# Optimization experiments

Measured on AMD Instinct MI355X. Metric: run time of the kernel, lower is better.

## Reference

```python
import jax, jax.numpy as jnp
import numpy as np

FACTOR = 8
IN_DIM = 4096
OUT_DIM = 4096


def setup_inputs() -> dict:
    key = jax.random.key(0)
    kx, ka, ks = jax.random.split(key, 3)
    x = jax.random.normal(kx, (4, 2048, IN_DIM), dtype=jnp.float32)
    a = jax.random.normal(ka, (FACTOR, FACTOR, FACTOR), dtype=jnp.float32) * 0.1
    s = jax.random.normal(ks, (FACTOR, OUT_DIM // FACTOR, IN_DIM // FACTOR), dtype=jnp.float32) * 0.05
    return {"x": x, "a": a, "s": s}


def reference(x, a, s):
    f = a.shape[0]
    out_dim = a.shape[1] * s.shape[1]
    in_dim = a.shape[2] * s.shape[2]
    # Batched Kronecker product: (f, a_rows*k, a_cols*p) then sum over batch dim f.
    # weight[a*k + ?, c*p + ?] = sum_b a[b, ar, ac] * s[b, kr, pc]
    p = jnp.einsum('bac,bkp->bakcp', a, s)  # (f, f, out/f, f, in/f)
    weight = p.reshape(f, out_dim, in_dim).sum(axis=0)  # (out, in)
    return x @ weight.T
```

## Files before the change

### kernel.cpp

```cpp
#include <hip/hip_runtime.h>
#include <hip/hip_bf16.h>
#include <stdint.h>

namespace {

constexpr int MTOT = 8192;
constexpr int NTOT = 4096;
constexpr int KTOT = 4096;

constexpr int BM = 256, BN = 128, BK = 32;
constexpr int NT = KTOT / BK;

typedef __attribute__((ext_vector_type(8))) short bf16x8;
typedef __attribute__((ext_vector_type(4))) float f32x4;

__device__ inline unsigned short to_bf16(float f) {
    union { float f; uint32_t u; } v; v.f = f;
    return (unsigned short)((v.u + 0x7FFFu + ((v.u >> 16) & 1u)) >> 16);
}

__global__ __launch_bounds__(256) void convert_x_kernel(const float* __restrict__ x,
                                                        unsigned short* __restrict__ xb) {
    int idx = blockIdx.x * 256 + threadIdx.x;
    const f32x4* xv = reinterpret_cast<const f32x4*>(x);
    f32x4 v0 = xv[2 * idx];
    f32x4 v1 = xv[2 * idx + 1];
    union { bf16x8 v; unsigned short s[8]; } o;
    o.s[0] = to_bf16(v0.x); o.s[1] = to_bf16(v0.y);
    o.s[2] = to_bf16(v0.z); o.s[3] = to_bf16(v0.w);
    o.s[4] = to_bf16(v1.x); o.s[5] = to_bf16(v1.y);
    o.s[6] = to_bf16(v1.z); o.s[7] = to_bf16(v1.w);
    reinterpret_cast<bf16x8*>(xb)[idx] = o.v;
}

__global__ __launch_bounds__(256) void gen_w_kernel(const float* __restrict__ a,
                                                    const float* __restrict__ s,
                                                    unsigned short* __restrict__ w) {
    int idx = blockIdx.x * 256 + threadIdx.x;
    int o  = idx >> 9;
    int i8 = idx & 511;
    int i0 = i8 * 8;
    int obig = o >> 9, orow = o & 511;
    int ibig = i0 >> 9, icol = i0 & 511;

    float acc[8];
#pragma unroll
    for (int j = 0; j < 8; ++j) acc[j] = 0.f;

#pragma unroll
    for (int b = 0; b < 8; ++b) {
        float av = a[b * 64 + obig * 8 + ibig];
        const f32x4* sv = reinterpret_cast<const f32x4*>(s + b * 512 * 512 + orow * 512 + icol);
        f32x4 s0 = sv[0], s1 = sv[1];
        acc[0] += av * s0.x; acc[1] += av * s0.y; acc[2] += av * s0.z; acc[3] += av * s0.w;
        acc[4] += av * s1.x; acc[5] += av * s1.y; acc[6] += av * s1.z; acc[7] += av * s1.w;
    }
    union { bf16x8 v; unsigned short q[8]; } ov;
#pragma unroll
    for (int j = 0; j < 8; ++j) ov.q[j] = to_bf16(acc[j]);
    reinterpret_cast<bf16x8*>(w)[idx] = ov.v;
}

__global__ __launch_bounds__(256, 2)
void gemm_bt_kernel(const unsigned short* __restrict__ A,
                    const unsigned short* __restrict__ B,
                    float* __restrict__ C) {
    __shared__ __align__(16) unsigned short As[3][BM][BK];
    __shared__ __align__(16) unsigned short Bs[3][BN][BK];

    int bid = blockIdx.x;
    int swz = (bid & 7) * 128 + (bid >> 3);
    int bm = swz >> 5;
    int bn = swz & 31;

    int tid  = threadIdx.x;
    int wid  = tid >> 6;
    int lane = tid & 63;
    int wm = wid >> 1, wn = wid & 1;

    int srow  = lane >> 2;
    int sslot = (lane & 3) ^ ((srow >> 1) & 3);
    const unsigned short* ag = A + (size_t)(bm * BM + wid * 64 + srow) * KTOT + sslot * 8;
    const unsigned short* bg = B + (size_t)(bn * BN + wid * 32 + srow) * KTOT + sslot * 8;

    int rl    = lane & 15;
    int rslot = (lane >> 4) ^ ((rl >> 1) & 3);

    f32x4 acc[8][4];
#pragma unroll
    for (int m = 0; m < 8; ++m)
#pragma unroll
        for (int n = 0; n < 4; ++n) acc[m][n] = (f32x4)0.f;

    auto STAGE = [&](int s, int k0) {
#pragma unroll
        for (int g = 0; g < 4; ++g)
            __builtin_amdgcn_global_load_lds(
                (const __attribute__((address_space(1))) void*)(ag + (size_t)g * 16 * KTOT + k0),
                (__attribute__((address_space(3))) void*)&As[s][wid * 64 + g * 16][0], 16, 0, 0);
#pragma unroll
        for (int g = 0; g < 2; ++g)
            __builtin_amdgcn_global_load_lds(
                (const __attribute__((address_space(1))) void*)(bg + (size_t)g * 16 * KTOT + k0),
                (__attribute__((address_space(3))) void*)&Bs[s][wid * 32 + g * 16][0], 16, 0, 0);
    };

    auto COMPUTE = [&](int s) {
        bf16x8 fa[8], fb[4];
#pragma unroll
        for (int m = 0; m < 8; ++m)
            fa[m] = *reinterpret_cast<const bf16x8*>(&As[s][wm * 128 + m * 16 + rl][rslot * 8]);
#pragma unroll
        for (int n = 0; n < 4; ++n)
            fb[n] = *reinterpret_cast<const bf16x8*>(&Bs[s][wn * 64 + n * 16 + rl][rslot * 8]);
        asm volatile("s_waitcnt lgkmcnt(0)" ::: "memory");
        __builtin_amdgcn_sched_barrier(0);
        __builtin_amdgcn_s_setprio(1);
#pragma unroll
        for (int m = 0; m < 8; ++m)
#pragma unroll
            for (int n = 0; n < 4; ++n)
                acc[m][n] = __builtin_amdgcn_mfma_f32_16x16x32_bf16(fa[m], fb[n], acc[m][n], 0, 0, 0);
        __builtin_amdgcn_s_setprio(0);
    };

    STAGE(0, 0);
    STAGE(1, BK);
    asm volatile("s_waitcnt vmcnt(6)" ::: "memory");
    __builtin_amdgcn_s_barrier();

    for (int tb = 0; tb < NT - 2; tb += 3) {
#pragma unroll
        for (int u = 0; u < 3; ++u) {
            const int t = tb + u;
            STAGE((u + 2) % 3, (t + 2) * BK);
            COMPUTE(u);
            asm volatile("s_waitcnt vmcnt(6)" ::: "memory");
            __builtin_amdgcn_s_barrier();
        }
    }
    COMPUTE(0);
    asm volatile("s_waitcnt vmcnt(0)" ::: "memory");
    __builtin_amdgcn_s_barrier();
    COMPUTE(1);

    int crow0 = bm * BM + wm * 128 + (lane >> 4) * 4;
    int ccol0 = bn * BN + wn * 64 + (lane & 15);
#pragma unroll
    for (int m = 0; m < 8; ++m)
#pragma unroll
        for (int n = 0; n < 4; ++n)
#pragma unroll
            for (int j = 0; j < 4; ++j) {
                size_t r = (size_t)(crow0 + m * 16 + j);
                size_t c = (size_t)(ccol0 + n * 16);
                C[r * NTOT + c] = acc[m][n][j];
            }
}

}

extern "C" void kernel_launch(void* const* d_in, const int* in_sizes, int n_in,
                              void* d_out, int out_size, void* d_ws, size_t ws_size,
                              hipStream_t stream) {
    const float* x = (const float*)d_in[0];
    const float* a = (const float*)d_in[1];
    const float* s = (const float*)d_in[2];
    float* out = (float*)d_out;

    unsigned short* xb = (unsigned short*)d_ws;
    unsigned short* wb = xb + (size_t)MTOT * KTOT;

    convert_x_kernel<<<(MTOT * KTOT / 8) / 256, 256, 0, stream>>>(x, xb);
    gen_w_kernel<<<(NTOT * KTOT / 8) / 256, 256, 0, stream>>>(a, s, wb);
    gemm_bt_kernel<<<(MTOT / BM) * (NTOT / BN), 256, 0, stream>>>(xb, wb, out);
}
```

Baseline: 326.9 us.

## Restructure GEMM into 256x256 tiles with 8 waves and interleaved ping-pong schedule

```diff
diff --git a/kernel.cpp b/kernel.cpp
--- a/kernel.cpp
+++ b/kernel.cpp
@@ -7,9 +7,6 @@
 constexpr int MTOT = 8192;
 constexpr int NTOT = 4096;
 constexpr int KTOT = 4096;
-
-constexpr int BM = 256, BN = 128, BK = 32;
-constexpr int NT = KTOT / BK;
 
 typedef __attribute__((ext_vector_type(8))) short bf16x8;
 typedef __attribute__((ext_vector_type(4))) float f32x4;
@@ -61,30 +58,62 @@
     reinterpret_cast<bf16x8*>(w)[idx] = ov.v;
 }
 
-__global__ __launch_bounds__(256, 2)
+__global__ __launch_bounds__(512, 2)
 void gemm_bt_kernel(const unsigned short* __restrict__ A,
                     const unsigned short* __restrict__ B,
                     float* __restrict__ C) {
-    __shared__ __align__(16) unsigned short As[3][BM][BK];
-    __shared__ __align__(16) unsigned short Bs[3][BN][BK];
+    __shared__ __align__(16) unsigned short As[2][2][128][64];
+    __shared__ __align__(16) unsigned short Bs[2][2][128][64];
 
     int bid = blockIdx.x;
-    int swz = (bid & 7) * 128 + (bid >> 3);
-    int bm = swz >> 5;
-    int bn = swz & 31;
+    int swz = (bid & 7) * 64 + (bid >> 3);
+    int bm = swz >> 4;
+    int bn = swz & 15;
 
     int tid  = threadIdx.x;
     int wid  = tid >> 6;
     int lane = tid & 63;
-    int wm = wid >> 1, wn = wid & 1;
-
-    int srow  = lane >> 2;
-    int sslot = (lane & 3) ^ ((srow >> 1) & 3);
-    const unsigned short* ag = A + (size_t)(bm * BM + wid * 64 + srow) * KTOT + sslot * 8;
-    const unsigned short* bg = B + (size_t)(bn * BN + wid * 32 + srow) * KTOT + sslot * 8;
-
-    int rl    = lane & 15;
-    int rslot = (lane >> 4) ^ ((rl >> 1) & 3);
+    int wm = wid >> 2, wn = wid & 3;
+
+    int r8 = lane >> 3;
+    int su = (lane & 7) ^ r8;
+    int rl = lane & 15;
+    int kq = lane >> 4;
+    int qx = rl & 7;
+
+    const size_t K = (size_t)KTOT;
+    const unsigned short* Abase = A + (size_t)(bm * 256 + wid * 16 + r8) * K + su * 8;
+    const unsigned short* Bbase = B + (size_t)(bn * 256 + wid * 16 + r8) * K + su * 8;
+
+    auto SA = [&](int buf, int h, int tile) {
+        const unsigned short* src = Abase + (size_t)(h * 128) * K + tile * 64;
+        __builtin_amdgcn_global_load_lds(
+            (const __attribute__((address_space(1))) void*)src,
+            (__attribute__((address_space(3))) void*)&As[buf][h][wid * 16][0], 16, 0, 0);
+        __builtin_amdgcn_global_load_lds(
+            (const __attribute__((address_space(1))) void*)(src + 8 * K),
+            (__attribute__((address_space(3))) void*)&As[buf][h][wid * 16 + 8][0], 16, 0, 0);
+    };
+    auto SB = [&](int buf, int h, int tile) {
+        const unsigned short* src = Bbase + (size_t)(h * 128) * K + tile * 64;
+        __builtin_amdgcn_global_load_lds(
+            (const __attribute__((address_space(1))) void*)src,
+            (__attribute__((address_space(3))) void*)&Bs[buf][h][wid * 16][0], 16, 0, 0);
+        __builtin_amdgcn_global_load_lds(
+            (const __attribute__((address_space(1))) void*)(src + 8 * K),
+            (__attribute__((address_space(3))) void*)&Bs[buf][h][wid * 16 + 8][0], 16, 0, 0);
+    };
+
+    auto LA = [&](int buf, int f, int ks) -> bf16x8 {
+        int rh = (f & 3) * 32 + wm * 16 + rl;
+        int q  = (ks * 4 + kq) ^ qx;
+        return *reinterpret_cast<const bf16x8*>(&As[buf][f >> 2][rh][q * 8]);
+    };
+    auto LB = [&](int buf, int g, int ks) -> bf16x8 {
+        int rh = (g & 1) * 64 + wn * 16 + rl;
+        int q  = (ks * 4 + kq) ^ qx;
+        return *reinterpret_cast<const bf16x8*>(&Bs[buf][g >> 1][rh][q * 8]);
+    };
 
     f32x4 acc[8][4];
 #pragma unroll
@@ -92,69 +121,88 @@
 #pragma unroll
         for (int n = 0; n < 4; ++n) acc[m][n] = (f32x4)0.f;
 
-    auto STAGE = [&](int s, int k0) {
-#pragma unroll
-        for (int g = 0; g < 4; ++g)
-            __builtin_amdgcn_global_load_lds(
-                (const __attribute__((address_space(1))) void*)(ag + (size_t)g * 16 * KTOT + k0),
-                (__attribute__((address_space(3))) void*)&As[s][wid * 64 + g * 16][0], 16, 0, 0);
-#pragma unroll
-        for (int g = 0; g < 2; ++g)
-            __builtin_amdgcn_global_load_lds(
-                (const __attribute__((address_space(1))) void*)(bg + (size_t)g * 16 * KTOT + k0),
-                (__attribute__((address_space(3))) void*)&Bs[s][wid * 32 + g * 16][0], 16, 0, 0);
-    };
-
-    auto COMPUTE = [&](int s) {
-        bf16x8 fa[8], fb[4];
-#pragma unroll
-        for (int m = 0; m < 8; ++m)
-            fa[m] = *reinterpret_cast<const bf16x8*>(&As[s][wm * 128 + m * 16 + rl][rslot * 8]);
-#pragma unroll
-        for (int n = 0; n < 4; ++n)
-            fb[n] = *reinterpret_cast<const bf16x8*>(&Bs[s][wn * 64 + n * 16 + rl][rslot * 8]);
+    bf16x8 a[4][2], bL[2][2], bH[2][2];
+
+    auto FENCE = [&]() {
+        __builtin_amdgcn_s_barrier();
         asm volatile("s_waitcnt lgkmcnt(0)" ::: "memory");
         __builtin_amdgcn_sched_barrier(0);
+    };
+    auto MM = [&](bf16x8 (&af)[4][2], bf16x8 (&bf)[2][2], int f0, int g0) {
         __builtin_amdgcn_s_setprio(1);
 #pragma unroll
-        for (int m = 0; m < 8; ++m)
-#pragma unroll
-            for (int n = 0; n < 4; ++n)
-                acc[m][n] = __builtin_amdgcn_mfma_f32_16x16x32_bf16(fa[m], fb[n], acc[m][n], 0, 0, 0);
+        for (int i = 0; i < 4; ++i)
+#pragma unroll
+            for (int gi = 0; gi < 2; ++gi)
+#pragma unroll
+                for (int ks = 0; ks < 2; ++ks)
+                    acc[f0 + i][g0 + gi] = __builtin_amdgcn_mfma_f32_16x16x32_bf16(
+                        af[i][ks], bf[gi][ks], acc[f0 + i][g0 + gi], 0, 0, 0);
         __builtin_amdgcn_s_setprio(0);
-    };
-
-    STAGE(0, 0);
-    STAGE(1, BK);
+        __builtin_amdgcn_s_barrier();
+    };
+
+    SA(0, 0, 0); SB(0, 0, 0); SB(0, 1, 0); SA(0, 1, 0);
+    SA(1, 0, 1); SB(1, 0, 1); SB(1, 1, 1);
     asm volatile("s_waitcnt vmcnt(6)" ::: "memory");
     __builtin_amdgcn_s_barrier();
 
-    for (int tb = 0; tb < NT - 2; tb += 3) {
-#pragma unroll
-        for (int u = 0; u < 3; ++u) {
-            const int t = tb + u;
-            STAGE((u + 2) % 3, (t + 2) * BK);
-            COMPUTE(u);
-            asm volatile("s_waitcnt vmcnt(6)" ::: "memory");
-            __builtin_amdgcn_s_barrier();
-        }
+    for (int j = 0; j < 32; ++j) {
+        const bool full = (j < 31);
+        const int t2 = 2 * j + 2, t3 = 2 * j + 3;
+
+#pragma unroll
+        for (int i = 0; i < 4; ++i) { a[i][0] = LA(0, i, 0); a[i][1] = LA(0, i, 1); }
+#pragma unroll
+        for (int gi = 0; gi < 2; ++gi) { bL[gi][0] = LB(0, gi, 0); bL[gi][1] = LB(0, gi, 1); }
+        SA(1, 1, 2 * j + 1);
+        FENCE(); MM(a, bL, 0, 0);
+
+#pragma unroll
+        for (int gi = 0; gi < 2; ++gi) { bH[gi][0] = LB(0, gi + 2, 0); bH[gi][1] = LB(0, gi + 2, 1); }
+        if (full) SA(0, 0, t2);
+        FENCE(); MM(a, bH, 0, 2);
+
+#pragma unroll
+        for (int i = 0; i < 4; ++i) { a[i][0] = LA(0, i + 4, 0); a[i][1] = LA(0, i + 4, 1); }
+        if (full) SB(0, 0, t2);
+        FENCE(); MM(a, bL, 4, 0);
+
+        if (full) { SB(0, 1, t2); asm volatile("s_waitcnt vmcnt(4)" ::: "memory"); }
+        else      {               asm volatile("s_waitcnt vmcnt(0)" ::: "memory"); }
+        FENCE(); MM(a, bH, 4, 2);
+
+#pragma unroll
+        for (int i = 0; i < 4; ++i) { a[i][0] = LA(1, i, 0); a[i][1] = LA(1, i, 1); }
+#pragma unroll
+        for (int gi = 0; gi < 2; ++gi) { bL[gi][0] = LB(1, gi, 0); bL[gi][1] = LB(1, gi, 1); }
+        if (full) SA(0, 1, t2);
+        FENCE(); MM(a, bL, 0, 0);
+
+#pragma unroll
+        for (int gi = 0; gi < 2; ++gi) { bH[gi][0] = LB(1, gi + 2, 0); bH[gi][1] = LB(1, gi + 2, 1); }
+        if (full) SA(1, 0, t3);
+        FENCE(); MM(a, bH, 0, 2);
+
+#pragma unroll
+        for (int i = 0; i < 4; ++i) { a[i][0] = LA(1, i + 4, 0); a[i][1] = LA(1, i + 4, 1); }
+        if (full) SB(1, 0, t3);
+        FENCE(); MM(a, bL, 4, 0);
+
+        if (full) { SB(1, 1, t3); asm volatile("s_waitcnt vmcnt(4)" ::: "memory"); }
+        FENCE(); MM(a, bH, 4, 2);
     }
-    COMPUTE(0);
-    asm volatile("s_waitcnt vmcnt(0)" ::: "memory");
-    __builtin_amdgcn_s_barrier();
-    COMPUTE(1);
-
-    int crow0 = bm * BM + wm * 128 + (lane >> 4) * 4;
-    int ccol0 = bn * BN + wn * 64 + (lane & 15);
-#pragma unroll
-    for (int m = 0; m < 8; ++m)
-#pragma unroll
-        for (int n = 0; n < 4; ++n)
-#pragma unroll
-            for (int j = 0; j < 4; ++j) {
-                size_t r = (size_t)(crow0 + m * 16 + j);
-                size_t c = (size_t)(ccol0 + n * 16);
-                C[r * NTOT + c] = acc[m][n][j];
+
+    int rq = (lane >> 4) * 4;
+#pragma unroll
+    for (int f = 0; f < 8; ++f)
+#pragma unroll
+        for (int g = 0; g < 4; ++g)
+#pragma unroll
+            for (int jj = 0; jj < 4; ++jj) {
+                size_t r = (size_t)(bm * 256 + (f & 3) * 32 + wm * 16 + (f >> 2) * 128 + rq + jj);
+                size_t c = (size_t)(bn * 256 + (g & 1) * 64 + wn * 16 + (g >> 1) * 128 + (lane & 15));
+                C[r * NTOT + c] = acc[f][g][jj];
             }
 }
 
@@ -173,5 +221,5 @@
 
     convert_x_kernel<<<(MTOT * KTOT / 8) / 256, 256, 0, stream>>>(x, xb);
     gen_w_kernel<<<(NTOT * KTOT / 8) / 256, 256, 0, stream>>>(a, s, wb);
-    gemm_bt_kernel<<<(MTOT / BM) * (NTOT / BN), 256, 0, stream>>>(xb, wb, out);
-}
+    gemm_bt_kernel<<<(MTOT / 256) * (NTOT / 256), 512, 0, stream>>>(xb, wb, out);
+}
```

New measurement: 323.9 us. No clear change (-0.9%).
